# Kernel optimization log

Hardware: AMD Instinct MI355X
Metric: run time of the kernel (lower is better)

The kernel has to match this reference:

```python
import jax, jax.numpy as jnp
import numpy as np

B, T, E, H = 4, 2048, 1024, 16
HS = E // H  # head_size = 64
FFN_HID = 100  # hard-coded in FeedForward
EPS = 1e-5


def layernorm(x, g, b):
    mu = jnp.mean(x, axis=-1, keepdims=True)
    var = jnp.mean(jnp.square(x - mu), axis=-1, keepdims=True)
    return (x - mu) * jax.lax.rsqrt(var + EPS) * g + b


def setup_inputs() -> dict:
    key = jax.random.key(0)
    ks = jax.random.split(key, 10)
    s = E ** -0.5
    return {
        "x": jax.random.normal(ks[0], (B, T, E), jnp.float32),
        "wq": jax.random.normal(ks[1], (E, E), jnp.float32) * s,
        "wk": jax.random.normal(ks[2], (E, E), jnp.float32) * s,
        "wv": jax.random.normal(ks[3], (E, E), jnp.float32) * s,
        "w_proj": jax.random.normal(ks[4], (E, E), jnp.float32) * s,
        "b_proj": jnp.zeros((E,), jnp.float32),
        "w1": jax.random.normal(ks[5], (E, FFN_HID), jnp.float32) * s,
        "b1": jnp.zeros((FFN_HID,), jnp.float32),
        "w2": jax.random.normal(ks[6], (FFN_HID, E), jnp.float32) * (FFN_HID ** -0.5),
        "b2": jnp.zeros((E,), jnp.float32),
        "ln1_g": jnp.ones((E,), jnp.float32),
        "ln1_b": jnp.zeros((E,), jnp.float32),
        "ln2_g": jnp.ones((E,), jnp.float32),
        "ln2_b": jnp.zeros((E,), jnp.float32),
    }


def reference(x, wq, wk, wv, w_proj, b_proj, w1, b1, w2, b2, ln1_g, ln1_b, ln2_g, ln2_b):
    # --- self-attention with pre-LN residual ---
    h = layernorm(x, ln1_g, ln1_b)  # [B,T,E]
    def split_heads(y):  # [B,T,E] -> [B,H,T,HS]
        return y.reshape(B, T, H, HS).transpose(0, 2, 1, 3)
    q = split_heads(h @ wq)
    k = split_heads(h @ wk)
    v = split_heads(h @ wv)
    # NOTE: original scales by C**-0.5 with C = n_embd (not head_size)
    wei = jnp.einsum("bhtd,bhsd->bhts", q, k) * (E ** -0.5)  # [B,H,T,T]
    causal = jnp.tril(jnp.ones((T, T), bool))
    wei = jnp.where(causal, wei, -jnp.inf)
    wei = jax.nn.softmax(wei, axis=-1)
    att = jnp.einsum("bhts,bhsd->bhtd", wei, v)  # [B,H,T,HS]
    att = att.transpose(0, 2, 1, 3).reshape(B, T, E)  # concat heads
    x = x + att @ w_proj + b_proj
    # --- feedforward with pre-LN residual ---
    h2 = layernorm(x, ln2_g, ln2_b)
    ff = jax.nn.relu(h2 @ w1 + b1) @ w2 + b2
    return x + ff
```

## Files before the change

kernel.cpp:

```cpp
#include <hip/hip_runtime.h>

typedef unsigned short u16;
typedef unsigned int u32;
typedef __bf16 bf16x8 __attribute__((ext_vector_type(8)));
typedef float f32x4 __attribute__((ext_vector_type(4)));

#define BDIM 4
#define TDIM 2048
#define EDIM 1024
#define HDIM 16
#define HS 64
#define MROWS (BDIM * TDIM)
#define FFNP 128

__device__ __forceinline__ u16 f2bf(float f) {
    __bf16 h = (__bf16)f;
    return __builtin_bit_cast(u16, h);
}

__device__ __forceinline__ void glds16(const void* g, void* l) {
    __builtin_amdgcn_global_load_lds(
        (__attribute__((address_space(1))) const void*)g,
        (__attribute__((address_space(3))) void*)l, 16, 0, 0);
}

__global__ __launch_bounds__(256) void transpose_all(
    const float* __restrict__ wq, const float* __restrict__ wk,
    const float* __restrict__ wv, const float* __restrict__ wproj,
    const float* __restrict__ w1, const float* __restrict__ w2,
    u16* __restrict__ wqkvt, u16* __restrict__ wpt,
    u16* __restrict__ w1t, u16* __restrict__ w2t)
{
    __shared__ u16 sm[64][72];
    const float* src; u16* dst;
    int K, N, Kpad, Npad;
    switch (blockIdx.z) {
        case 0: src = wq;    dst = wqkvt;                 K = N = Kpad = Npad = 1024; break;
        case 1: src = wk;    dst = wqkvt + 1024 * 1024;   K = N = Kpad = Npad = 1024; break;
        case 2: src = wv;    dst = wqkvt + 2 * 1024 * 1024; K = N = Kpad = Npad = 1024; break;
        case 3: src = wproj; dst = wpt;                   K = N = Kpad = Npad = 1024; break;
        case 4: src = w1;    dst = w1t; K = 1024; N = 100; Kpad = 1024; Npad = 128; break;
        default: src = w2;   dst = w2t; K = 100; N = 1024; Kpad = 128; Npad = 1024; break;
    }
    int k0 = blockIdx.x * 64, n0 = blockIdx.y * 64;
    if (k0 >= Kpad || n0 >= Npad) return;
    int tid = threadIdx.x;
#pragma unroll
    for (int i = 0; i < 16; i++) {
        int idx = i * 256 + tid;
        int kl = idx >> 6, nl = idx & 63;
        int k = k0 + kl, n = n0 + nl;
        float v = (k < K && n < N) ? src[(size_t)k * N + n] : 0.f;
        sm[kl][nl] = f2bf(v);
    }
    __syncthreads();
#pragma unroll
    for (int i = 0; i < 16; i++) {
        int idx = i * 256 + tid;
        int nl = idx >> 6, kl = idx & 63;
        int n = n0 + nl, k = k0 + kl;
        if (n < Npad && k < Kpad) dst[(size_t)n * Kpad + k] = sm[kl][nl];
    }
}

__global__ __launch_bounds__(256) void ln_rows(
    const float* __restrict__ X, const float* __restrict__ G,
    const float* __restrict__ Bv, u16* __restrict__ H)
{
    int w = threadIdx.x >> 6, l = threadIdx.x & 63;
    int row = blockIdx.x * 4 + w;
    const float* xr = X + (size_t)row * EDIM;
    float4 v[4];
    float s = 0.f, s2 = 0.f;
#pragma unroll
    for (int i = 0; i < 4; i++) {
        v[i] = *(const float4*)&xr[l * 4 + i * 256];
        s += v[i].x + v[i].y + v[i].z + v[i].w;
        s2 += v[i].x * v[i].x + v[i].y * v[i].y + v[i].z * v[i].z + v[i].w * v[i].w;
    }
#pragma unroll
    for (int off = 1; off < 64; off <<= 1) {
        s += __shfl_xor(s, off, 64);
        s2 += __shfl_xor(s2, off, 64);
    }
    float mean = s * (1.f / EDIM);
    float var = s2 * (1.f / EDIM) - mean * mean;
    float rstd = rsqrtf(var + 1e-5f);
#pragma unroll
    for (int i = 0; i < 4; i++) {
        int c = l * 4 + i * 256;
        float4 gg = *(const float4*)&G[c];
        float4 bb = *(const float4*)&Bv[c];
        u16 o0 = f2bf((v[i].x - mean) * rstd * gg.x + bb.x);
        u16 o1 = f2bf((v[i].y - mean) * rstd * gg.y + bb.y);
        u16 o2 = f2bf((v[i].z - mean) * rstd * gg.z + bb.z);
        u16 o3 = f2bf((v[i].w - mean) * rstd * gg.w + bb.w);
        uint2 pk;
        pk.x = (u32)o0 | ((u32)o1 << 16);
        pk.y = (u32)o2 | ((u32)o3 << 16);
        *(uint2*)&H[(size_t)row * EDIM + c] = pk;
    }
}

#define LDA4(d, mfb)                                                          \
    _Pragma("unroll") for (int mi = 0; mi < 4; mi++)                          \
    _Pragma("unroll") for (int ks = 0; ks < 2; ks++)                          \
        a[mi][ks] = *(const bf16x8*)&L[d][0][wm][((mfb + mi) * 16 + lr) * 64  \
                        + (((lg + 4 * ks) ^ (lr & 7)) << 3)];
#define LDB2(d, nfb)                                                          \
    _Pragma("unroll") for (int ni = 0; ni < 2; ni++)                          \
    _Pragma("unroll") for (int ks = 0; ks < 2; ks++)                          \
        b[ni][ks] = *(const bf16x8*)&L[d][1][wh][((wn & 1) * 64               \
                        + (nfb + ni) * 16 + lr) * 64                          \
                        + (((lg + 4 * ks) ^ (lr & 7)) << 3)];
#define MFMAQ(mfb, nfb)                                                       \
    _Pragma("unroll") for (int mi = 0; mi < 4; mi++)                          \
    _Pragma("unroll") for (int ni = 0; ni < 2; ni++)                          \
    _Pragma("unroll") for (int ks = 0; ks < 2; ks++)                          \
        acc[mfb + mi][nfb + ni] = __builtin_amdgcn_mfma_f32_16x16x32_bf16(    \
            a[mi][ks], b[ni][ks], acc[mfb + mi][nfb + ni], 0, 0, 0);
#define PH_SYNC1()                                                            \
    __builtin_amdgcn_s_barrier();                                             \
    asm volatile("s_waitcnt lgkmcnt(0)" ::: "memory");                        \
    __builtin_amdgcn_sched_barrier(0);                                        \
    __builtin_amdgcn_s_setprio(1);
#define PH_SYNC2()                                                            \
    __builtin_amdgcn_s_setprio(0);                                            \
    __builtin_amdgcn_s_barrier();
#define PH_SYNC2V(cond)                                                       \
    __builtin_amdgcn_s_setprio(0);                                            \
    if (cond) { asm volatile("s_waitcnt vmcnt(2)" ::: "memory"); }            \
    else      { asm volatile("s_waitcnt vmcnt(0)" ::: "memory"); }            \
    __builtin_amdgcn_s_barrier();

__global__ __launch_bounds__(512, 2) void gemm256_qk(
    const u16* __restrict__ A, const u16* __restrict__ Bt,
    u16* __restrict__ Cb)
{
    __shared__ u16 L[2][2][2][128 * 64];
    int id = blockIdx.x;
    int sw = (id & 7) * 32 + (id >> 3);
    int bx = sw % 32, by = sw / 32;
    const int m0 = bx * 256, n0 = by * 256;

    const int tid = threadIdx.x;
    const int w = tid >> 6, l = tid & 63;
    const int wm = w >> 2, wn = w & 3, wh = wn >> 1;
    const int lg = l >> 4, lr = l & 15;

    const int srow = w * 16 + (l >> 3);
    const int sch8 = ((l & 7) ^ (l >> 3)) * 8;

    auto stA = [&](int d, int h, int t) {
        const u16* src = A + (size_t)(m0 + h * 128 + srow) * 1024 + t * 64 + sch8;
        u16* dst = &L[d][0][h][w * 1024];
        glds16(src, dst);
        glds16(src + (size_t)8 * 1024, dst + 512);
    };
    auto stB = [&](int d, int h, int t) {
        const u16* src = Bt + (size_t)(n0 + h * 128 + srow) * 1024 + t * 64 + sch8;
        u16* dst = &L[d][1][h][w * 1024];
        glds16(src, dst);
        glds16(src + (size_t)8 * 1024, dst + 512);
    };

    f32x4 acc[8][4];
#pragma unroll
    for (int i = 0; i < 8; i++)
#pragma unroll
        for (int j = 0; j < 4; j++) acc[i][j] = f32x4{0.f, 0.f, 0.f, 0.f};
    bf16x8 a[4][2], b[2][2];

    const int NI = 1024 >> 7;

    stA(0, 0, 0); stA(0, 1, 0); stB(0, 0, 0); stB(0, 1, 0);
    stB(1, 0, 1);
    asm volatile("s_waitcnt vmcnt(2)" ::: "memory");
    __builtin_amdgcn_s_barrier();

#pragma unroll 1
    for (int j = 0; j < NI; j++) {
        const int t = 2 * j;
        const bool more = (j + 1 < NI);
        LDA4(0, 0); LDB2(0, 0);
        stA(1, 0, t + 1);
        PH_SYNC1(); MFMAQ(0, 0); PH_SYNC2();
        LDA4(0, 4);
        stA(1, 1, t + 1);
        PH_SYNC1(); MFMAQ(4, 0); PH_SYNC2();
        LDB2(0, 2);
        stB(1, 1, t + 1);
        PH_SYNC1(); MFMAQ(4, 2); PH_SYNC2();
        LDA4(0, 0);
        if (more) stB(0, 1, t + 2);
        PH_SYNC1(); MFMAQ(0, 2); PH_SYNC2V(more);
        LDA4(1, 0); LDB2(1, 0);
        if (more) stA(0, 0, t + 2);
        PH_SYNC1(); MFMAQ(0, 0); PH_SYNC2();
        LDA4(1, 4);
        if (more) stA(0, 1, t + 2);
        PH_SYNC1(); MFMAQ(4, 0); PH_SYNC2();
        LDB2(1, 2);
        if (more) stB(0, 0, t + 2);
        PH_SYNC1(); MFMAQ(4, 2); PH_SYNC2();
        LDA4(1, 0);
        if (more) stB(1, 0, t + 3);
        PH_SYNC1(); MFMAQ(0, 2); PH_SYNC2V(more);
    }

#pragma unroll
    for (int mf = 0; mf < 8; mf++) {
#pragma unroll
        for (int nf = 0; nf < 4; nf++) {
#pragma unroll
            for (int e = 0; e < 4; e++) {
                int row = m0 + wm * 128 + mf * 16 + lg * 4 + e;
                int col = n0 + wn * 64 + nf * 16 + lr;
                Cb[(size_t)row * 2048 + col] = f2bf(acc[mf][nf][e]);
            }
        }
    }
}

template <int MODE>
__global__ __launch_bounds__(256, 2) void gemm_bt(
    const u16* __restrict__ A, const u16* __restrict__ Bt,
    float* __restrict__ Cf,
    const float* __restrict__ resid, const float* __restrict__ bias,
    int M, int N, int K, int lda, int ldb, int mb)
{
    __shared__ u16 As[2][128 * 32];
    __shared__ u16 Bs[2][128 * 32];
    int bx, by;
    if constexpr (MODE == 4) {
        bx = blockIdx.x; by = blockIdx.y;
        int kz = blockIdx.z;
        A += kz * 256;
        Bt += kz * 256;
        Cf += (size_t)kz * M * N;
    } else {
        int nwg = gridDim.x, id = blockIdx.x;
        int sw = (id & 7) * (nwg >> 3) + (id >> 3);
        bx = sw % mb; by = sw / mb;
    }
    const int tid = threadIdx.x;
    const int w = tid >> 6, l = tid & 63;
    const int wr = w >> 1, wc = w & 1;
    const int lg = l >> 4, lr = l & 15;
    const int m0 = bx * 128, n0 = by * 128;

    f32x4 zero = {0.f, 0.f, 0.f, 0.f};
    f32x4 acc[4][4];
#pragma unroll
    for (int i = 0; i < 4; i++)
#pragma unroll
        for (int j = 0; j < 4; j++) acc[i][j] = zero;

    const u16* Ag = A + (size_t)(m0 + w * 16 + (l >> 2)) * lda + (l & 3) * 8;
    const u16* Bg = Bt + (size_t)(n0 + w * 16 + (l >> 2)) * ldb + (l & 3) * 8;

    auto stage = [&](int b, int k0) {
        glds16(Ag + k0, &As[b][w * 512]);
        glds16(Ag + k0 + (size_t)64 * lda, &As[b][w * 512 + 2048]);
        glds16(Bg + k0, &Bs[b][w * 512]);
        glds16(Bg + k0 + (size_t)64 * ldb, &Bs[b][w * 512 + 2048]);
    };
    auto compute = [&](int b) {
        bf16x8 af[4], bfr[4];
#pragma unroll
        for (int t = 0; t < 4; t++)
            af[t] = *(const bf16x8*)&As[b][(wr * 64 + t * 16 + lr) * 32 + lg * 8];
#pragma unroll
        for (int t = 0; t < 4; t++)
            bfr[t] = *(const bf16x8*)&Bs[b][(wc * 64 + t * 16 + lr) * 32 + lg * 8];
#pragma unroll
        for (int i = 0; i < 4; i++)
#pragma unroll
            for (int j = 0; j < 4; j++)
                acc[i][j] = __builtin_amdgcn_mfma_f32_16x16x32_bf16(
                    af[i], bfr[j], acc[i][j], 0, 0, 0);
    };

    stage(0, 0);
    __syncthreads();
    int cur = 0;
    for (int k0 = 32; k0 < K; k0 += 32) {
        stage(cur ^ 1, k0);
        compute(cur);
        __syncthreads();
        cur ^= 1;
    }
    compute(cur);

#pragma unroll
    for (int i = 0; i < 4; i++) {
#pragma unroll
        for (int j = 0; j < 4; j++) {
#pragma unroll
            for (int e = 0; e < 4; e++) {
                int row = m0 + wr * 64 + i * 16 + lg * 4 + e;
                int col = n0 + wc * 64 + j * 16 + lr;
                float v = acc[i][j][e];
                if constexpr (MODE == 1 || MODE == 3) {
                    size_t idx = (size_t)row * N + col;
                    Cf[idx] = resid[idx] + v + bias[col];
                } else if constexpr (MODE == 4) {
                    Cf[(size_t)row * N + col] = v;
                } else {
                    u16* vtp = (u16*)Cf;
                    int bq = col >> 11, tt = col & 2047;
                    vtp[((size_t)bq * 1024 + row) * 2048 + tt] = f2bf(v);
                }
            }
        }
    }
}

__global__ __launch_bounds__(256) void relu_reduce4(
    const float* __restrict__ fp, const float* __restrict__ b1,
    u16* __restrict__ tb)
{
    const size_t CH = (size_t)MROWS * FFNP;
    size_t base = ((size_t)blockIdx.x * 256 + threadIdx.x) * 4;
    float4 s0 = *(const float4*)&fp[base];
    float4 s1 = *(const float4*)&fp[base + CH];
    float4 s2 = *(const float4*)&fp[base + 2 * CH];
    float4 s3 = *(const float4*)&fp[base + 3 * CH];
    int col = (int)(base & (FFNP - 1));
    float sv[4] = {s0.x + s1.x + s2.x + s3.x, s0.y + s1.y + s2.y + s3.y,
                   s0.z + s1.z + s2.z + s3.z, s0.w + s1.w + s2.w + s3.w};
    u16 o[4];
#pragma unroll
    for (int j = 0; j < 4; j++) {
        int c = col + j;
        float b = (c < 100) ? b1[c] : 0.f;
        o[j] = f2bf(fmaxf(sv[j] + b, 0.f));
    }
    uint2 pk;
    pk.x = (u32)o[0] | ((u32)o[1] << 16);
    pk.y = (u32)o[2] | ((u32)o[3] << 16);
    *(uint2*)&tb[base] = pk;
}

__global__ __launch_bounds__(256, 4) void attn_fwd(
    const u16* __restrict__ qk, const u16* __restrict__ Vt,
    u16* __restrict__ Og)
{
    int xcd = blockIdx.x & 7;
    int j = blockIdx.x >> 3;
    int bh = xcd * 8 + (j & 7);
    int qp = j >> 3;
    int bb = bh >> 4, hh = bh & 15;

    int tid = threadIdx.x;
    int w = tid >> 6, l = tid & 63;
    int lg = l >> 4, lr = l & 15;

    const u16* Qb = qk + ((size_t)bb * TDIM) * 2048 + hh * HS;
    const u16* Kb = Qb + 1024;
    const u16* Vb = Vt + (size_t)bh * HS * TDIM;

    __shared__ u16 Ks[2][64 * 64];
    __shared__ u16 Vs[2][64 * 64];
    __shared__ __align__(16) u16 Ps[4][16 * 64];

    int srow = w * 16 + (l >> 3);
    int schunk = (l & 7) ^ ((l >> 3) & 7);
    u16* Pw = Ps[w];
    int sbase = (l & 48) + lg * 4;

    const float QSCL = 0.045084227f;

#pragma unroll 1
    for (int qi = 0; qi < 2; qi++) {
        int qb = (qi == 0 ? qp : 31 - qp) * 64;
        int q_abs = qb + w * 16 + lr;
        int wlo = qb + w * 16;
        int nt = qb / 64 + 1;

        bf16x8 qf[2];
        qf[0] = *(const bf16x8*)&Qb[(size_t)q_abs * 2048 + lg * 8];
        qf[1] = *(const bf16x8*)&Qb[(size_t)q_abs * 2048 + 32 + lg * 8];
#pragma unroll
        for (int i = 0; i < 8; i++) {
            qf[0][i] = (__bf16)((float)qf[0][i] * QSCL);
            qf[1][i] = (__bf16)((float)qf[1][i] * QSCL);
        }

        f32x4 zero = {0.f, 0.f, 0.f, 0.f};
        f32x4 oacc[4];
#pragma unroll
        for (int dt = 0; dt < 4; dt++) oacc[dt] = zero;
        float lpart = 0.f;

        auto stage = [&](int b, int kv0) {
            glds16(Kb + (size_t)(kv0 + srow) * 2048 + schunk * 8, &Ks[b][w * 1024]);
            glds16(Kb + (size_t)(kv0 + srow + 8) * 2048 + schunk * 8,
                   &Ks[b][w * 1024 + 512]);
            glds16(Vb + (size_t)srow * TDIM + kv0 + schunk * 8, &Vs[b][w * 1024]);
            glds16(Vb + (size_t)(srow + 8) * TDIM + kv0 + schunk * 8,
                   &Vs[b][w * 1024 + 512]);
        };

        stage(0, 0);
        if (nt > 1) stage(1, 64);
#pragma unroll 1
        for (int t = 0; t < nt; t++) {
            int kv0 = t * 64;
            int buf = t & 1;
            if (t + 1 < nt) { asm volatile("s_waitcnt vmcnt(4)" ::: "memory"); }
            else            { asm volatile("s_waitcnt vmcnt(0)" ::: "memory"); }
            __builtin_amdgcn_sched_barrier(0);
            __builtin_amdgcn_s_barrier();
            const u16* Kc = Ks[buf];
            const u16* Vc = Vs[buf];
            f32x4 sc[4];
#pragma unroll
            for (int ct = 0; ct < 4; ct++) sc[ct] = zero;
            __builtin_amdgcn_s_setprio(1);
#pragma unroll
            for (int ct = 0; ct < 4; ct++) {
#pragma unroll
                for (int dc = 0; dc < 2; dc++) {
                    bf16x8 kf = *(const bf16x8*)&Kc[(ct * 16 + lr) * 64 +
                                                    (((lg + 4 * dc) ^ (lr & 7)) << 3)];
                    sc[ct] = __builtin_amdgcn_mfma_f32_16x16x32_bf16(
                        kf, qf[dc], sc[ct], 0, 0, 0);
                }
            }
            __builtin_amdgcn_s_setprio(0);
            bf16x8 vfr[2][4];
#pragma unroll
            for (int m = 0; m < 2; m++)
#pragma unroll
                for (int dt = 0; dt < 4; dt++)
                    vfr[m][dt] = *(const bf16x8*)&Vc[(dt * 16 + lr) * 64 +
                                                     (((lg + 4 * m) ^ (lr & 7)) << 3)];
            float p[16];
            if (kv0 + 63 > wlo) {
#pragma unroll
                for (int ct = 0; ct < 4; ct++) {
#pragma unroll
                    for (int e = 0; e < 4; e++) {
                        float v = sc[ct][e];
                        if (kv0 + ct * 16 + lg * 4 + e > q_abs) v = -1e30f;
                        p[ct * 4 + e] = v;
                    }
                }
            } else {
#pragma unroll
                for (int ct = 0; ct < 4; ct++) {
#pragma unroll
                    for (int e = 0; e < 4; e++) p[ct * 4 + e] = sc[ct][e];
                }
            }
            float psum = 0.f;
#pragma unroll
            for (int i = 0; i < 16; i++) {
                p[i] = __builtin_amdgcn_exp2f(p[i]);
                psum += p[i];
            }
            lpart += psum;
#pragma unroll
            for (int ct = 0; ct < 4; ct++) {
                uint2 pr;
                pr.x = (u32)f2bf(p[ct * 4 + 0]) | ((u32)f2bf(p[ct * 4 + 1]) << 16);
                pr.y = (u32)f2bf(p[ct * 4 + 2]) | ((u32)f2bf(p[ct * 4 + 3]) << 16);
                int kvb = ct * 16 + lg * 4;
                int idx = lr * 64 + ((((kvb >> 3) ^ (lr & 7)) << 3) | (kvb & 7));
                *(uint2*)&Pw[idx] = pr;
            }
            asm volatile("s_waitcnt lgkmcnt(0)" ::: "memory");
            __builtin_amdgcn_sched_barrier(0);
            __builtin_amdgcn_s_setprio(1);
#pragma unroll
            for (int m = 0; m < 2; m++) {
                bf16x8 pa = *(const bf16x8*)&Pw[lr * 64 + (((lg + 4 * m) ^ (lr & 7)) << 3)];
#pragma unroll
                for (int dt = 0; dt < 4; dt++) {
                    oacc[dt] = __builtin_amdgcn_mfma_f32_16x16x32_bf16(
                        pa, vfr[m][dt], oacc[dt], 0, 0, 0);
                }
            }
            __builtin_amdgcn_s_setprio(0);
            __builtin_amdgcn_s_barrier();
            if (t + 2 < nt) stage(buf, kv0 + 128);
        }
        float lsum = lpart;
        lsum += __shfl_xor(lsum, 16, 64);
        lsum += __shfl_xor(lsum, 32, 64);
        float lT[4];
#pragma unroll
        for (int e = 0; e < 4; e++) lT[e] = __shfl(lsum, sbase + e, 64);
#pragma unroll
        for (int dt = 0; dt < 4; dt++) {
#pragma unroll
            for (int e = 0; e < 4; e++) {
                int row = qb + w * 16 + lg * 4 + e;
                Og[((size_t)bb * TDIM + row) * EDIM + hh * HS + dt * 16 + lr] =
                    f2bf(oacc[dt][e] / lT[e]);
            }
        }
    }
}

extern "C" void kernel_launch(void* const* d_in, const int* in_sizes, int n_in,
                              void* d_out, int out_size, void* d_ws, size_t ws_size,
                              hipStream_t stream)
{
    const float* x     = (const float*)d_in[0];
    const float* wq    = (const float*)d_in[1];
    const float* wk    = (const float*)d_in[2];
    const float* wv    = (const float*)d_in[3];
    const float* wproj = (const float*)d_in[4];
    const float* bproj = (const float*)d_in[5];
    const float* w1    = (const float*)d_in[6];
    const float* b1    = (const float*)d_in[7];
    const float* w2    = (const float*)d_in[8];
    const float* b2    = (const float*)d_in[9];
    const float* ln1g  = (const float*)d_in[10];
    const float* ln1b  = (const float*)d_in[11];
    const float* ln2g  = (const float*)d_in[12];
    const float* ln2b  = (const float*)d_in[13];
    float* out = (float*)d_out;

    char* ws = (char*)d_ws;
    size_t off = 0;
    auto alloc = [&](size_t bytes) -> void* {
        void* p = (void*)(ws + off);
        off += (bytes + 255) & ~(size_t)255;
        return p;
    };
    u16* hbuf = (u16*)alloc((size_t)MROWS * EDIM * 2);
    u16* qk   = (u16*)alloc((size_t)MROWS * 2048 * 2);
    u16* attb = (u16*)alloc((size_t)MROWS * EDIM * 2);
    u16* vt   = (u16*)alloc((size_t)MROWS * EDIM * 2);
    u16* wqkvt = (u16*)alloc((size_t)3072 * EDIM * 2);
    u16* wpt  = (u16*)alloc((size_t)EDIM * EDIM * 2);
    u16* w1t  = (u16*)alloc((size_t)FFNP * EDIM * 2);
    u16* w2t  = (u16*)alloc((size_t)EDIM * FFNP * 2);
    float* fp = (float*)qk;
    u16* tb   = vt;

    transpose_all<<<dim3(16, 16, 6), 256, 0, stream>>>(
        wq, wk, wv, wproj, w1, w2, wqkvt, wpt, w1t, w2t);

    ln_rows<<<MROWS / 4, 256, 0, stream>>>(x, ln1g, ln1b, hbuf);
    gemm256_qk<<<dim3(256), 512, 0, stream>>>(hbuf, wqkvt, qk);
    gemm_bt<5><<<dim3(512), 256, 0, stream>>>(wqkvt + (size_t)2048 * 1024, hbuf,
                                              (float*)vt, nullptr, nullptr,
                                              1024, 8192, 1024, 1024, 1024, 8);
    attn_fwd<<<dim3(1024), 256, 0, stream>>>(qk, vt, attb);
    gemm_bt<1><<<dim3(512), 256, 0, stream>>>(attb, wpt, out, x, bproj,
                                              MROWS, EDIM, EDIM, EDIM, EDIM, 64);
    ln_rows<<<MROWS / 4, 256, 0, stream>>>(out, ln2g, ln2b, hbuf);
    gemm_bt<4><<<dim3(64, 1, 4), 256, 0, stream>>>(hbuf, w1t, fp, nullptr, nullptr,
                                                   MROWS, FFNP, 256, EDIM, EDIM, 64);
    relu_reduce4<<<dim3(MROWS * FFNP / 1024), 256, 0, stream>>>(fp, b1, tb);
    gemm_bt<3><<<dim3(512), 256, 0, stream>>>(tb, w2t, out, out, b2,
                                              MROWS, EDIM, FFNP, FFNP, FFNP, 64);
}
```

Measured before the change: 216.5 us.

## Split attention QK^T across waves by key columns, share P tile in LDS

Changes the attention work split. Each wave now loads its own 16-key slice of K once and computes scores against all 64 query rows held in registers, instead of reading all 64 keys per wave. This cuts LDS reads of K. The probability tile moves into a block-shared LDS buffer, which needs an extra barrier before PV, and the row sums are reduced across waves through LDS that reuses the K buffer. The tradeoff is more Q registers, more block-wide synchronisation, and masking applied only on the diagonal tile.

Measured after the change: 258.2 us. +19.2%, slower.

```diff
diff --git a/kernel.cpp b/kernel.cpp
--- a/kernel.cpp
+++ b/kernel.cpp
@@ -362,36 +362,37 @@
 
     __shared__ u16 Ks[2][64 * 64];
     __shared__ u16 Vs[2][64 * 64];
-    __shared__ __align__(16) u16 Ps[4][16 * 64];
+    __shared__ __align__(16) u16 Ps[64 * 64];
+    float* Ls = (float*)&Ks[0][0];
 
     int srow = w * 16 + (l >> 3);
     int schunk = (l & 7) ^ ((l >> 3) & 7);
-    u16* Pw = Ps[w];
-    int sbase = (l & 48) + lg * 4;
 
     const float QSCL = 0.045084227f;
 
 #pragma unroll 1
     for (int qi = 0; qi < 2; qi++) {
         int qb = (qi == 0 ? qp : 31 - qp) * 64;
-        int q_abs = qb + w * 16 + lr;
-        int wlo = qb + w * 16;
         int nt = qb / 64 + 1;
 
-        bf16x8 qf[2];
-        qf[0] = *(const bf16x8*)&Qb[(size_t)q_abs * 2048 + lg * 8];
-        qf[1] = *(const bf16x8*)&Qb[(size_t)q_abs * 2048 + 32 + lg * 8];
-#pragma unroll
-        for (int i = 0; i < 8; i++) {
-            qf[0][i] = (__bf16)((float)qf[0][i] * QSCL);
-            qf[1][i] = (__bf16)((float)qf[1][i] * QSCL);
+        bf16x8 qfb[4][2];
+#pragma unroll
+        for (int qc = 0; qc < 4; qc++) {
+            size_t qrow = (size_t)(qb + qc * 16 + lr) * 2048;
+            qfb[qc][0] = *(const bf16x8*)&Qb[qrow + lg * 8];
+            qfb[qc][1] = *(const bf16x8*)&Qb[qrow + 32 + lg * 8];
+#pragma unroll
+            for (int i = 0; i < 8; i++) {
+                qfb[qc][0][i] = (__bf16)((float)qfb[qc][0][i] * QSCL);
+                qfb[qc][1][i] = (__bf16)((float)qfb[qc][1][i] * QSCL);
+            }
         }
 
         f32x4 zero = {0.f, 0.f, 0.f, 0.f};
         f32x4 oacc[4];
 #pragma unroll
         for (int dt = 0; dt < 4; dt++) oacc[dt] = zero;
-        float lpart = 0.f;
+        float lp[4] = {0.f, 0.f, 0.f, 0.f};
 
         auto stage = [&](int b, int kv0) {
             glds16(Kb + (size_t)(kv0 + srow) * 2048 + schunk * 8, &Ks[b][w * 1024]);
@@ -414,20 +415,21 @@
             __builtin_amdgcn_s_barrier();
             const u16* Kc = Ks[buf];
             const u16* Vc = Vs[buf];
+            bf16x8 kf[2];
+#pragma unroll
+            for (int dc = 0; dc < 2; dc++)
+                kf[dc] = *(const bf16x8*)&Kc[(w * 16 + lr) * 64 +
+                                             (((lg + 4 * dc) ^ (lr & 7)) << 3)];
             f32x4 sc[4];
 #pragma unroll
-            for (int ct = 0; ct < 4; ct++) sc[ct] = zero;
+            for (int qc = 0; qc < 4; qc++) sc[qc] = zero;
             __builtin_amdgcn_s_setprio(1);
 #pragma unroll
-            for (int ct = 0; ct < 4; ct++) {
-#pragma unroll
-                for (int dc = 0; dc < 2; dc++) {
-                    bf16x8 kf = *(const bf16x8*)&Kc[(ct * 16 + lr) * 64 +
-                                                    (((lg + 4 * dc) ^ (lr & 7)) << 3)];
-                    sc[ct] = __builtin_amdgcn_mfma_f32_16x16x32_bf16(
-                        kf, qf[dc], sc[ct], 0, 0, 0);
-                }
-            }
+            for (int qc = 0; qc < 4; qc++)
+#pragma unroll
+                for (int dc = 0; dc < 2; dc++)
+                    sc[qc] = __builtin_amdgcn_mfma_f32_16x16x32_bf16(
+                        kf[dc], qfb[qc][dc], sc[qc], 0, 0, 0);
             __builtin_amdgcn_s_setprio(0);
             bf16x8 vfr[2][4];
 #pragma unroll
@@ -436,46 +438,33 @@
                 for (int dt = 0; dt < 4; dt++)
                     vfr[m][dt] = *(const bf16x8*)&Vc[(dt * 16 + lr) * 64 +
                                                      (((lg + 4 * m) ^ (lr & 7)) << 3)];
-            float p[16];
-            if (kv0 + 63 > wlo) {
-#pragma unroll
-                for (int ct = 0; ct < 4; ct++) {
-#pragma unroll
-                    for (int e = 0; e < 4; e++) {
-                        float v = sc[ct][e];
-                        if (kv0 + ct * 16 + lg * 4 + e > q_abs) v = -1e30f;
-                        p[ct * 4 + e] = v;
-                    }
+            const bool diag = (t == nt - 1);
+            int kvbase = kv0 + w * 16 + lg * 4;
+            int pcol = ((((w * 16 + lg * 4) >> 3) ^ (lr & 7)) << 3) | ((lg * 4) & 7);
+#pragma unroll
+            for (int qc = 0; qc < 4; qc++) {
+                float pv[4];
+#pragma unroll
+                for (int e = 0; e < 4; e++) {
+                    float v = sc[qc][e];
+                    if (diag && (kvbase + e > qb + qc * 16 + lr)) v = -1e30f;
+                    pv[e] = __builtin_amdgcn_exp2f(v);
                 }
-            } else {
-#pragma unroll
-                for (int ct = 0; ct < 4; ct++) {
-#pragma unroll
-                    for (int e = 0; e < 4; e++) p[ct * 4 + e] = sc[ct][e];
-                }
-            }
-            float psum = 0.f;
-#pragma unroll
-            for (int i = 0; i < 16; i++) {
-                p[i] = __builtin_amdgcn_exp2f(p[i]);
-                psum += p[i];
-            }
-            lpart += psum;
-#pragma unroll
-            for (int ct = 0; ct < 4; ct++) {
+                lp[qc] += pv[0] + pv[1] + pv[2] + pv[3];
                 uint2 pr;
-                pr.x = (u32)f2bf(p[ct * 4 + 0]) | ((u32)f2bf(p[ct * 4 + 1]) << 16);
-                pr.y = (u32)f2bf(p[ct * 4 + 2]) | ((u32)f2bf(p[ct * 4 + 3]) << 16);
-                int kvb = ct * 16 + lg * 4;
-                int idx = lr * 64 + ((((kvb >> 3) ^ (lr & 7)) << 3) | (kvb & 7));
-                *(uint2*)&Pw[idx] = pr;
+                pr.x = (u32)f2bf(pv[0]) | ((u32)f2bf(pv[1]) << 16);
+                pr.y = (u32)f2bf(pv[2]) | ((u32)f2bf(pv[3]) << 16);
+                *(uint2*)&Ps[(qc * 16 + lr) * 64 + pcol] = pr;
             }
             asm volatile("s_waitcnt lgkmcnt(0)" ::: "memory");
             __builtin_amdgcn_sched_barrier(0);
+            __builtin_amdgcn_s_barrier();
+            if (t + 2 < nt) stage(buf, kv0 + 128);
             __builtin_amdgcn_s_setprio(1);
 #pragma unroll
             for (int m = 0; m < 2; m++) {
-                bf16x8 pa = *(const bf16x8*)&Pw[lr * 64 + (((lg + 4 * m) ^ (lr & 7)) << 3)];
+                bf16x8 pa = *(const bf16x8*)&Ps[(w * 16 + lr) * 64 +
+                                                (((lg + 4 * m) ^ (lr & 7)) << 3)];
 #pragma unroll
                 for (int dt = 0; dt < 4; dt++) {
                     oacc[dt] = __builtin_amdgcn_mfma_f32_16x16x32_bf16(
@@ -483,15 +472,25 @@
                 }
             }
             __builtin_amdgcn_s_setprio(0);
-            __builtin_amdgcn_s_barrier();
-            if (t + 2 < nt) stage(buf, kv0 + 128);
-        }
-        float lsum = lpart;
-        lsum += __shfl_xor(lsum, 16, 64);
-        lsum += __shfl_xor(lsum, 32, 64);
+        }
+#pragma unroll
+        for (int qc = 0; qc < 4; qc++) {
+            lp[qc] += __shfl_xor(lp[qc], 16, 64);
+            lp[qc] += __shfl_xor(lp[qc], 32, 64);
+        }
+        if (lg == 0) {
+#pragma unroll
+            for (int qc = 0; qc < 4; qc++)
+                Ls[(qc * 16 + lr) * 4 + w] = lp[qc];
+        }
+        asm volatile("s_waitcnt lgkmcnt(0)" ::: "memory");
+        __builtin_amdgcn_s_barrier();
         float lT[4];
 #pragma unroll
-        for (int e = 0; e < 4; e++) lT[e] = __shfl(lsum, sbase + e, 64);
+        for (int e = 0; e < 4; e++) {
+            float4 lv = *(const float4*)&Ls[(w * 16 + lg * 4 + e) * 4];
+            lT[e] = (lv.x + lv.y) + (lv.z + lv.w);
+        }
 #pragma unroll
         for (int dt = 0; dt < 4; dt++) {
 #pragma unroll
@@ -501,6 +500,7 @@
                     f2bf(oacc[dt][e] / lT[e]);
             }
         }
+        __builtin_amdgcn_s_barrier();
     }
 }
 
```
